# Performance work log

Measured on AMD Instinct MI355X. Metric: run time of the kernel, lower is better.

Reference implementation:

```python
import jax, jax.numpy as jnp
import numpy as np

B, TE, TD, H, D = 8, 2048, 256, 128, 128


def setup_inputs() -> dict:
    key = jax.random.key(0)
    k1, k2, k3, k4, k5 = jax.random.split(key, 5)
    he = lambda k, shape: jax.random.normal(k, shape, dtype=jnp.float32) * jnp.sqrt(2.0 / shape[0])
    return {
        "encoder_out_seq": jax.random.normal(k1, (B, TE, H), dtype=jnp.float32),
        "decoder_out_seq": jax.random.normal(k2, (B, TD, D), dtype=jnp.float32),
        "W_a": he(k3, (H, H)),
        "U_a": he(k4, (D, H)),
        "V_a": he(k5, (H, 1)),
    }


def reference(encoder_out_seq, decoder_out_seq, W_a, U_a, V_a):
    # Precompute encoder and decoder projections once (the TF code redundantly
    # recomputes enc@W_a every decoder step inside backend.rnn).
    Wenc = jnp.einsum('bth,hk->btk', encoder_out_seq, W_a)      # [B,Te,H]
    Udec = jnp.einsum('bjd,dk->bjk', decoder_out_seq, U_a)     # [B,Td,H]
    # Additive (Bahdanau) scores: v^T tanh(W s_i + U h_j)
    scores = jnp.einsum('bjtk,k->bjt',
                        jnp.tanh(Wenc[:, None, :, :] + Udec[:, :, None, :]),
                        V_a[:, 0])                              # [B,Td,Te]
    e_outputs = jax.nn.softmax(scores, axis=-1)                 # [B,Td,Te]
    c_outputs = jnp.einsum('bjt,bth->bjh', e_outputs, encoder_out_seq)  # [B,Td,H]
    return c_outputs, e_outputs
```

## Files before the change

kernel.cpp:

```cpp
#include <hip/hip_runtime.h>
#include <stdint.h>

#define B  8
#define TE 2048
#define TD 256
#define H  128

#define FMA4(acc, s, wv) \
  acc.x += (s)*(wv).x; acc.y += (s)*(wv).y; acc.z += (s)*(wv).z; acc.w += (s)*(wv).w

__global__ __launch_bounds__(256) void proj_kernel(
    const float* __restrict__ enc, const float* __restrict__ dec,
    const float* __restrict__ Wa,  const float* __restrict__ Ua,
    float* __restrict__ EgT, float* __restrict__ Fg) {
  __shared__ float Ls[16 * 132];
  const float C2 = 2.8853900817779268f;
  int tid = threadIdx.x;
  int bid = blockIdx.x;
  bool isE = (bid < 1024);
  int rbase = (isE ? bid : bid - 1024) * 16;
  const float* in = isE ? enc : dec;
  const float* Mg = isE ? Wa : Ua;
  int hq = tid & 31, rq = tid >> 5;
  int h0 = hq * 4, r0 = rq * 2;
  const float* rowp = in + (size_t)(rbase + r0) * H;
  const float* wp = Mg + h0;
  float4 a0{0,0,0,0}, a1{0,0,0,0};
  #pragma unroll 2
  for (int kb = 0; kb < 32; ++kb) {
    float4 rv0 = *(const float4*)(rowp + kb * 4);
    float4 rv1 = *(const float4*)(rowp + H + kb * 4);
    float4 w0 = *(const float4*)(wp + (size_t)(4 * kb + 0) * H);
    float4 w1 = *(const float4*)(wp + (size_t)(4 * kb + 1) * H);
    float4 w2 = *(const float4*)(wp + (size_t)(4 * kb + 2) * H);
    float4 w3 = *(const float4*)(wp + (size_t)(4 * kb + 3) * H);
    FMA4(a0, rv0.x, w0); FMA4(a0, rv0.y, w1); FMA4(a0, rv0.z, w2); FMA4(a0, rv0.w, w3);
    FMA4(a1, rv1.x, w0); FMA4(a1, rv1.y, w1); FMA4(a1, rv1.z, w2); FMA4(a1, rv1.w, w3);
  }
  float4 e0, e1;
  e0.x = __builtin_amdgcn_exp2f(a0.x * C2); e0.y = __builtin_amdgcn_exp2f(a0.y * C2);
  e0.z = __builtin_amdgcn_exp2f(a0.z * C2); e0.w = __builtin_amdgcn_exp2f(a0.w * C2);
  e1.x = __builtin_amdgcn_exp2f(a1.x * C2); e1.y = __builtin_amdgcn_exp2f(a1.y * C2);
  e1.z = __builtin_amdgcn_exp2f(a1.z * C2); e1.w = __builtin_amdgcn_exp2f(a1.w * C2);
  if (isE) {
    *(float4*)&Ls[(r0 + 0) * 132 + h0] = e0;
    *(float4*)&Ls[(r0 + 1) * 132 + h0] = e1;
    __syncthreads();
    int b_e = rbase >> 11, t_in = rbase & 2047;
    int tb = t_in >> 6, toff = t_in & 63;
    float* dst = EgT + ((size_t)(b_e * 32 + tb) * 128) * 64 + toff;
    #pragma unroll
    for (int jj = 0; jj < 8; ++jj) {
      int idx = jj * 256 + tid;
      int r = idx & 15, k = idx >> 4;
      dst[(size_t)k * 64 + r] = Ls[r * 132 + k];
    }
  } else {
    int b_f = rbase >> 8, j_in = rbase & 255;
    float* dst = Fg + ((size_t)(b_f * TD + j_in + r0)) * H + h0;
    *(float4*)(dst + 0 * H) = e0;
    *(float4*)(dst + 1 * H) = e1;
  }
}

__global__ __launch_bounds__(512, 4) void fused_kernel(
    const float* __restrict__ EgT, const float* __restrict__ Fg,
    const float* __restrict__ Va,  const float* __restrict__ enc,
    float* __restrict__ oute, float* __restrict__ outc) {
  __shared__ float S[4 * 2048];
  __shared__ float red[16];
  int tid = threadIdx.x;
  int bid = blockIdx.x;
  int b = bid & 7, jt = bid >> 3;
  int j0 = jt * 4;
  int lane = tid & 63, w = tid >> 6;
  const float4* vp = (const float4*)Va;
  float V1 = 0.f;
  #pragma unroll
  for (int q = 0; q < 32; ++q) { float4 v = vp[q]; V1 += v.x + v.y + v.z + v.w; }

  const float4* Fp = (const float4*)(Fg + (size_t)(b * TD + j0) * H);
  const float* Ep[4];
  #pragma unroll
  for (int it = 0; it < 4; ++it)
    Ep[it] = EgT + ((size_t)(b * 32 + w + 8 * it) * 128) * 64 + lane;
  float s[4][4];
  #pragma unroll
  for (int it = 0; it < 4; ++it)
    #pragma unroll
    for (int j = 0; j < 4; ++j) s[it][j] = 0.f;

  for (int kc = 0; kc < 16; ++kc) {
    float4 f0[4], f1[4];
    const float4* fpc = Fp + kc * 2;
    #pragma unroll
    for (int j = 0; j < 4; ++j) {
      f0[j] = fpc[j * 32];
      f1[j] = fpc[j * 32 + 1];
    }
    float4 v0 = vp[kc * 2], v1 = vp[kc * 2 + 1];
    #pragma unroll
    for (int it = 0; it < 4; ++it) {
      const float* ep = Ep[it] + kc * 512;
      float ek[8];
      #pragma unroll
      for (int q = 0; q < 8; ++q) ek[q] = ep[q * 64];
      #pragma unroll
      for (int j = 0; j < 4; ++j) {
        float d0, d1, a = 0.f;
        d0 = fmaf(ek[0], f0[j].x, 1.0f); d1 = fmaf(ek[1], f0[j].y, 1.0f);
        a += (v0.x * d1 + v0.y * d0) * __builtin_amdgcn_rcpf(d0 * d1);
        d0 = fmaf(ek[2], f0[j].z, 1.0f); d1 = fmaf(ek[3], f0[j].w, 1.0f);
        a += (v0.z * d1 + v0.w * d0) * __builtin_amdgcn_rcpf(d0 * d1);
        d0 = fmaf(ek[4], f1[j].x, 1.0f); d1 = fmaf(ek[5], f1[j].y, 1.0f);
        a += (v1.x * d1 + v1.y * d0) * __builtin_amdgcn_rcpf(d0 * d1);
        d0 = fmaf(ek[6], f1[j].z, 1.0f); d1 = fmaf(ek[7], f1[j].w, 1.0f);
        a += (v1.z * d1 + v1.w * d0) * __builtin_amdgcn_rcpf(d0 * d1);
        s[it][j] += a;
      }
    }
  }
  #pragma unroll
  for (int it = 0; it < 4; ++it) {
    int t = (w + 8 * it) * 64 + lane;
    S[0 * 2048 + t] = V1 - 2.0f * s[it][0];
    S[1 * 2048 + t] = V1 - 2.0f * s[it][1];
    S[2 * 2048 + t] = V1 - 2.0f * s[it][2];
    S[3 * 2048 + t] = V1 - 2.0f * s[it][3];
  }
  __syncthreads();

  int j = w >> 1, half = w & 1;
  int tb2 = half * 1024 + lane;
  float x[16];
  #pragma unroll
  for (int q = 0; q < 16; ++q) x[q] = S[j * 2048 + tb2 + q * 64];
  float m = x[0];
  #pragma unroll
  for (int q = 1; q < 16; ++q) m = fmaxf(m, x[q]);
  #pragma unroll
  for (int off = 32; off > 0; off >>= 1) m = fmaxf(m, __shfl_xor(m, off));
  if (lane == 0) red[w] = m;
  __syncthreads();
  m = fmaxf(red[j * 2], red[j * 2 + 1]);
  const float L2E = 1.4426950408889634f;
  float sum = 0.f;
  #pragma unroll
  for (int q = 0; q < 16; ++q) {
    x[q] = __builtin_amdgcn_exp2f((x[q] - m) * L2E);
    sum += x[q];
  }
  #pragma unroll
  for (int off = 32; off > 0; off >>= 1) sum += __shfl_xor(sum, off);
  if (lane == 0) red[8 + w] = sum;
  __syncthreads();
  float inv = 1.0f / (red[8 + j * 2] + red[8 + j * 2 + 1]);
  float* orow = oute + (size_t)(b * TD + j0 + j) * TE;
  #pragma unroll
  for (int q = 0; q < 16; ++q) {
    float e = x[q] * inv;
    int t = tb2 + q * 64;
    orow[t] = e;
    S[t * 4 + j] = e;
  }
  __syncthreads();

  int hq = tid & 31, slice = tid >> 5;
  const float* encp = enc + ((size_t)b * TE + slice * 128) * H + hq * 4;
  float4 acc0{0,0,0,0}, acc1{0,0,0,0}, acc2{0,0,0,0}, acc3{0,0,0,0};
  #pragma unroll 4
  for (int t = 0; t < 128; ++t) {
    float4 ev = *(const float4*)(encp + (size_t)t * H);
    float4 e4 = *(const float4*)&S[(slice * 128 + t) * 4];
    acc0.x += e4.x * ev.x; acc0.y += e4.x * ev.y; acc0.z += e4.x * ev.z; acc0.w += e4.x * ev.w;
    acc1.x += e4.y * ev.x; acc1.y += e4.y * ev.y; acc1.z += e4.y * ev.z; acc1.w += e4.y * ev.w;
    acc2.x += e4.z * ev.x; acc2.y += e4.z * ev.y; acc2.z += e4.z * ev.z; acc2.w += e4.z * ev.w;
    acc3.x += e4.w * ev.x; acc3.y += e4.w * ev.y; acc3.z += e4.w * ev.z; acc3.w += e4.w * ev.w;
  }
  __syncthreads();
  *(float4*)&S[slice * 512 + 0 * 128 + hq * 4] = acc0;
  *(float4*)&S[slice * 512 + 1 * 128 + hq * 4] = acc1;
  *(float4*)&S[slice * 512 + 2 * 128 + hq * 4] = acc2;
  *(float4*)&S[slice * 512 + 3 * 128 + hq * 4] = acc3;
  __syncthreads();
  float r = 0.f;
  #pragma unroll
  for (int sl = 0; sl < 16; ++sl) r += S[sl * 512 + tid];
  outc[(size_t)(b * TD + j0 + (tid >> 7)) * H + (tid & 127)] = r;
}

extern "C" void kernel_launch(void* const* d_in, const int* in_sizes, int n_in,
                              void* d_out, int out_size, void* d_ws, size_t ws_size,
                              hipStream_t stream) {
  (void)in_sizes; (void)n_in; (void)out_size; (void)ws_size;
  const float* enc = (const float*)d_in[0];
  const float* dec = (const float*)d_in[1];
  const float* Wa  = (const float*)d_in[2];
  const float* Ua  = (const float*)d_in[3];
  const float* Va  = (const float*)d_in[4];

  float* ws  = (float*)d_ws;
  float* EgT = ws;
  float* Fg  = EgT + (size_t)B * TE * H;
  float* outc = (float*)d_out;
  float* oute = outc + (size_t)B * TD * H;

  proj_kernel<<<dim3(1152), 256, 0, stream>>>(enc, dec, Wa, Ua, EgT, Fg);
  fused_kernel<<<dim3(512), 512, 0, stream>>>(EgT, Fg, Va, enc, oute, outc);
}
```

Before: 168.8 us.

## Process eight decoder rows per block with 1024 threads in fused attention kernel

```diff
diff --git a/kernel.cpp b/kernel.cpp
--- a/kernel.cpp
+++ b/kernel.cpp
@@ -63,16 +63,16 @@
   }
 }
 
-__global__ __launch_bounds__(512, 4) void fused_kernel(
+__global__ __launch_bounds__(1024, 4) void fused_kernel(
     const float* __restrict__ EgT, const float* __restrict__ Fg,
     const float* __restrict__ Va,  const float* __restrict__ enc,
     float* __restrict__ oute, float* __restrict__ outc) {
-  __shared__ float S[4 * 2048];
-  __shared__ float red[16];
+  __shared__ float S[8 * 2048];
+  __shared__ float red[32];
   int tid = threadIdx.x;
   int bid = blockIdx.x;
   int b = bid & 7, jt = bid >> 3;
-  int j0 = jt * 4;
+  int j0 = jt * 8;
   int lane = tid & 63, w = tid >> 6;
   const float4* vp = (const float4*)Va;
   float V1 = 0.f;
@@ -80,53 +80,56 @@
   for (int q = 0; q < 32; ++q) { float4 v = vp[q]; V1 += v.x + v.y + v.z + v.w; }
 
   const float4* Fp = (const float4*)(Fg + (size_t)(b * TD + j0) * H);
-  const float* Ep[4];
-  #pragma unroll
-  for (int it = 0; it < 4; ++it)
-    Ep[it] = EgT + ((size_t)(b * 32 + w + 8 * it) * 128) * 64 + lane;
-  float s[4][4];
-  #pragma unroll
-  for (int it = 0; it < 4; ++it)
-    #pragma unroll
-    for (int j = 0; j < 4; ++j) s[it][j] = 0.f;
+  const float* Ep0 = EgT + ((size_t)(b * 32 + w) * 128) * 64 + lane;
+  const float* Ep1 = EgT + ((size_t)(b * 32 + w + 16) * 128) * 64 + lane;
+  float s0[8], s1[8];
+  #pragma unroll
+  for (int j = 0; j < 8; ++j) { s0[j] = 0.f; s1[j] = 0.f; }
+
+#define UNIT(acc, ekk, jj)                                                \
+  {                                                                       \
+    float d0, d1, a = 0.f;                                                \
+    d0 = fmaf(ekk[0], f0[jj].x, 1.0f); d1 = fmaf(ekk[1], f0[jj].y, 1.0f); \
+    a += (v0.x * d1 + v0.y * d0) * __builtin_amdgcn_rcpf(d0 * d1);        \
+    d0 = fmaf(ekk[2], f0[jj].z, 1.0f); d1 = fmaf(ekk[3], f0[jj].w, 1.0f); \
+    a += (v0.z * d1 + v0.w * d0) * __builtin_amdgcn_rcpf(d0 * d1);        \
+    d0 = fmaf(ekk[4], f1[jj].x, 1.0f); d1 = fmaf(ekk[5], f1[jj].y, 1.0f); \
+    a += (v1.x * d1 + v1.y * d0) * __builtin_amdgcn_rcpf(d0 * d1);        \
+    d0 = fmaf(ekk[6], f1[jj].z, 1.0f); d1 = fmaf(ekk[7], f1[jj].w, 1.0f); \
+    a += (v1.z * d1 + v1.w * d0) * __builtin_amdgcn_rcpf(d0 * d1);        \
+    acc[jj] += a;                                                         \
+  }
 
   for (int kc = 0; kc < 16; ++kc) {
-    float4 f0[4], f1[4];
+    float4 f0[8], f1[8];
     const float4* fpc = Fp + kc * 2;
     #pragma unroll
-    for (int j = 0; j < 4; ++j) {
+    for (int j = 0; j < 8; ++j) {
       f0[j] = fpc[j * 32];
       f1[j] = fpc[j * 32 + 1];
     }
     float4 v0 = vp[kc * 2], v1 = vp[kc * 2 + 1];
-    #pragma unroll
-    for (int it = 0; it < 4; ++it) {
-      const float* ep = Ep[it] + kc * 512;
+    {
+      const float* ep = Ep0 + kc * 512;
       float ek[8];
       #pragma unroll
       for (int q = 0; q < 8; ++q) ek[q] = ep[q * 64];
       #pragma unroll
-      for (int j = 0; j < 4; ++j) {
-        float d0, d1, a = 0.f;
-        d0 = fmaf(ek[0], f0[j].x, 1.0f); d1 = fmaf(ek[1], f0[j].y, 1.0f);
-        a += (v0.x * d1 + v0.y * d0) * __builtin_amdgcn_rcpf(d0 * d1);
-        d0 = fmaf(ek[2], f0[j].z, 1.0f); d1 = fmaf(ek[3], f0[j].w, 1.0f);
-        a += (v0.z * d1 + v0.w * d0) * __builtin_amdgcn_rcpf(d0 * d1);
-        d0 = fmaf(ek[4], f1[j].x, 1.0f); d1 = fmaf(ek[5], f1[j].y, 1.0f);
-        a += (v1.x * d1 + v1.y * d0) * __builtin_amdgcn_rcpf(d0 * d1);
-        d0 = fmaf(ek[6], f1[j].z, 1.0f); d1 = fmaf(ek[7], f1[j].w, 1.0f);
-        a += (v1.z * d1 + v1.w * d0) * __builtin_amdgcn_rcpf(d0 * d1);
-        s[it][j] += a;
-      }
-    }
-  }
-  #pragma unroll
-  for (int it = 0; it < 4; ++it) {
-    int t = (w + 8 * it) * 64 + lane;
-    S[0 * 2048 + t] = V1 - 2.0f * s[it][0];
-    S[1 * 2048 + t] = V1 - 2.0f * s[it][1];
-    S[2 * 2048 + t] = V1 - 2.0f * s[it][2];
-    S[3 * 2048 + t] = V1 - 2.0f * s[it][3];
+      for (int j = 0; j < 8; ++j) UNIT(s0, ek, j)
+    }
+    {
+      const float* ep = Ep1 + kc * 512;
+      float ek[8];
+      #pragma unroll
+      for (int q = 0; q < 8; ++q) ek[q] = ep[q * 64];
+      #pragma unroll
+      for (int j = 0; j < 8; ++j) UNIT(s1, ek, j)
+    }
+  }
+  #pragma unroll
+  for (int j = 0; j < 8; ++j) {
+    S[j * 2048 + w * 64 + lane]        = V1 - 2.0f * s0[j];
+    S[j * 2048 + (w + 16) * 64 + lane] = V1 - 2.0f * s1[j];
   }
   __syncthreads();
 
@@ -152,40 +155,56 @@
   }
   #pragma unroll
   for (int off = 32; off > 0; off >>= 1) sum += __shfl_xor(sum, off);
-  if (lane == 0) red[8 + w] = sum;
-  __syncthreads();
-  float inv = 1.0f / (red[8 + j * 2] + red[8 + j * 2 + 1]);
+  if (lane == 0) red[16 + w] = sum;
+  __syncthreads();
+  float inv = 1.0f / (red[16 + j * 2] + red[16 + j * 2 + 1]);
   float* orow = oute + (size_t)(b * TD + j0 + j) * TE;
   #pragma unroll
   for (int q = 0; q < 16; ++q) {
     float e = x[q] * inv;
     int t = tb2 + q * 64;
     orow[t] = e;
-    S[t * 4 + j] = e;
+    S[j * 2048 + t] = e;
   }
   __syncthreads();
 
   int hq = tid & 31, slice = tid >> 5;
-  const float* encp = enc + ((size_t)b * TE + slice * 128) * H + hq * 4;
-  float4 acc0{0,0,0,0}, acc1{0,0,0,0}, acc2{0,0,0,0}, acc3{0,0,0,0};
-  #pragma unroll 4
-  for (int t = 0; t < 128; ++t) {
+  const float* encp = enc + ((size_t)b * TE + slice * 64) * H + hq * 4;
+  const float* Se = S + slice * 64;
+  float4 ac0{0,0,0,0}, ac1{0,0,0,0}, ac2{0,0,0,0}, ac3{0,0,0,0};
+  float4 ac4{0,0,0,0}, ac5{0,0,0,0}, ac6{0,0,0,0}, ac7{0,0,0,0};
+  #pragma unroll 2
+  for (int t = 0; t < 64; ++t) {
     float4 ev = *(const float4*)(encp + (size_t)t * H);
-    float4 e4 = *(const float4*)&S[(slice * 128 + t) * 4];
-    acc0.x += e4.x * ev.x; acc0.y += e4.x * ev.y; acc0.z += e4.x * ev.z; acc0.w += e4.x * ev.w;
-    acc1.x += e4.y * ev.x; acc1.y += e4.y * ev.y; acc1.z += e4.y * ev.z; acc1.w += e4.y * ev.w;
-    acc2.x += e4.z * ev.x; acc2.y += e4.z * ev.y; acc2.z += e4.z * ev.z; acc2.w += e4.z * ev.w;
-    acc3.x += e4.w * ev.x; acc3.y += e4.w * ev.y; acc3.z += e4.w * ev.z; acc3.w += e4.w * ev.w;
-  }
-  __syncthreads();
-  *(float4*)&S[slice * 512 + 0 * 128 + hq * 4] = acc0;
-  *(float4*)&S[slice * 512 + 1 * 128 + hq * 4] = acc1;
-  *(float4*)&S[slice * 512 + 2 * 128 + hq * 4] = acc2;
-  *(float4*)&S[slice * 512 + 3 * 128 + hq * 4] = acc3;
+    float e0v = Se[0 * 2048 + t], e1v = Se[1 * 2048 + t];
+    float e2v = Se[2 * 2048 + t], e3v = Se[3 * 2048 + t];
+    float e4v = Se[4 * 2048 + t], e5v = Se[5 * 2048 + t];
+    float e6v = Se[6 * 2048 + t], e7v = Se[7 * 2048 + t];
+    FMA4(ac0, e0v, ev); FMA4(ac1, e1v, ev); FMA4(ac2, e2v, ev); FMA4(ac3, e3v, ev);
+    FMA4(ac4, e4v, ev); FMA4(ac5, e5v, ev); FMA4(ac6, e6v, ev); FMA4(ac7, e7v, ev);
+  }
+  __syncthreads();
+  if (slice < 16) {
+    float* dst = &S[slice * 1024 + hq * 4];
+    *(float4*)(dst + 0 * 128) = ac0; *(float4*)(dst + 1 * 128) = ac1;
+    *(float4*)(dst + 2 * 128) = ac2; *(float4*)(dst + 3 * 128) = ac3;
+    *(float4*)(dst + 4 * 128) = ac4; *(float4*)(dst + 5 * 128) = ac5;
+    *(float4*)(dst + 6 * 128) = ac6; *(float4*)(dst + 7 * 128) = ac7;
+  }
+  __syncthreads();
+  if (slice >= 16) {
+    float* dst = &S[(slice - 16) * 1024 + hq * 4];
+    #define RMW(J, AC) { float4 p = *(float4*)(dst + J * 128); \
+      p.x += AC.x; p.y += AC.y; p.z += AC.z; p.w += AC.w; \
+      *(float4*)(dst + J * 128) = p; }
+    RMW(0, ac0) RMW(1, ac1) RMW(2, ac2) RMW(3, ac3)
+    RMW(4, ac4) RMW(5, ac5) RMW(6, ac6) RMW(7, ac7)
+    #undef RMW
+  }
   __syncthreads();
   float r = 0.f;
   #pragma unroll
-  for (int sl = 0; sl < 16; ++sl) r += S[sl * 512 + tid];
+  for (int sl = 0; sl < 16; ++sl) r += S[sl * 1024 + tid];
   outc[(size_t)(b * TD + j0 + (tid >> 7)) * H + (tid & 127)] = r;
 }
 
@@ -206,5 +225,5 @@
   float* oute = outc + (size_t)B * TD * H;
 
   proj_kernel<<<dim3(1152), 256, 0, stream>>>(enc, dec, Wa, Ua, EgT, Fg);
-  fused_kernel<<<dim3(512), 512, 0, stream>>>(EgT, Fg, Va, enc, oute, outc);
+  fused_kernel<<<dim3(256), 1024, 0, stream>>>(EgT, Fg, Va, enc, oute, outc);
 }
```

Measured after the change: 169.9 us. Within noise of the previous version (+0.6%).

## Prefetch encoder tiles, merge reciprocals, and restructure context accumulation layout

Applied to the files above, without the earlier changes.

```diff
diff --git a/kernel.cpp b/kernel.cpp
--- a/kernel.cpp
+++ b/kernel.cpp
@@ -89,7 +89,26 @@
   for (int it = 0; it < 4; ++it)
     #pragma unroll
     for (int j = 0; j < 4; ++j) s[it][j] = 0.f;
-
+  float eka[8], ekb[8];
+
+#define LOADE(dst, base, off)                                        \
+  { const float* _p = (base) + (off);                                \
+    dst[0] = _p[0];   dst[1] = _p[64];  dst[2] = _p[128];            \
+    dst[3] = _p[192]; dst[4] = _p[256]; dst[5] = _p[320];            \
+    dst[6] = _p[384]; dst[7] = _p[448]; }
+
+#define UNIT4(accres, e0_, e1_, e2_, e3_, fv, vv)                         \
+  {                                                                       \
+    float d0 = fmaf(e0_, fv.x, 1.0f), d1 = fmaf(e1_, fv.y, 1.0f);        \
+    float d2 = fmaf(e2_, fv.z, 1.0f), d3 = fmaf(e3_, fv.w, 1.0f);        \
+    float p01 = d0 * d1, p23 = d2 * d3;                                   \
+    float rP = __builtin_amdgcn_rcpf(p01 * p23);                          \
+    float n01 = vv.x * d1 + vv.y * d0;                                    \
+    float n23 = vv.z * d3 + vv.w * d2;                                    \
+    accres = fmaf(n01 * p23 + n23 * p01, rP, accres);                     \
+  }
+
+  LOADE(eka, Ep[0], 0);
   for (int kc = 0; kc < 16; ++kc) {
     float4 f0[4], f1[4];
     const float4* fpc = Fp + kc * 2;
@@ -101,23 +120,15 @@
     float4 v0 = vp[kc * 2], v1 = vp[kc * 2 + 1];
     #pragma unroll
     for (int it = 0; it < 4; ++it) {
-      const float* ep = Ep[it] + kc * 512;
-      float ek[8];
-      #pragma unroll
-      for (int q = 0; q < 8; ++q) ek[q] = ep[q * 64];
+      if (it < 3) { LOADE(ekb, Ep[it + 1], kc * 512); }
+      else        { LOADE(ekb, Ep[0], (kc + 1) * 512); }
       #pragma unroll
       for (int j = 0; j < 4; ++j) {
-        float d0, d1, a = 0.f;
-        d0 = fmaf(ek[0], f0[j].x, 1.0f); d1 = fmaf(ek[1], f0[j].y, 1.0f);
-        a += (v0.x * d1 + v0.y * d0) * __builtin_amdgcn_rcpf(d0 * d1);
-        d0 = fmaf(ek[2], f0[j].z, 1.0f); d1 = fmaf(ek[3], f0[j].w, 1.0f);
-        a += (v0.z * d1 + v0.w * d0) * __builtin_amdgcn_rcpf(d0 * d1);
-        d0 = fmaf(ek[4], f1[j].x, 1.0f); d1 = fmaf(ek[5], f1[j].y, 1.0f);
-        a += (v1.x * d1 + v1.y * d0) * __builtin_amdgcn_rcpf(d0 * d1);
-        d0 = fmaf(ek[6], f1[j].z, 1.0f); d1 = fmaf(ek[7], f1[j].w, 1.0f);
-        a += (v1.z * d1 + v1.w * d0) * __builtin_amdgcn_rcpf(d0 * d1);
-        s[it][j] += a;
+        UNIT4(s[it][j], eka[0], eka[1], eka[2], eka[3], f0[j], v0);
+        UNIT4(s[it][j], eka[4], eka[5], eka[6], eka[7], f1[j], v1);
       }
+      #pragma unroll
+      for (int q = 0; q < 8; ++q) eka[q] = ekb[q];
     }
   }
   #pragma unroll
@@ -161,31 +172,61 @@
     float e = x[q] * inv;
     int t = tb2 + q * 64;
     orow[t] = e;
-    S[t * 4 + j] = e;
+    S[j * 2048 + t] = e;
   }
   __syncthreads();
 
   int hq = tid & 31, slice = tid >> 5;
   const float* encp = enc + ((size_t)b * TE + slice * 128) * H + hq * 4;
-  float4 acc0{0,0,0,0}, acc1{0,0,0,0}, acc2{0,0,0,0}, acc3{0,0,0,0};
-  #pragma unroll 4
-  for (int t = 0; t < 128; ++t) {
-    float4 ev = *(const float4*)(encp + (size_t)t * H);
-    float4 e4 = *(const float4*)&S[(slice * 128 + t) * 4];
-    acc0.x += e4.x * ev.x; acc0.y += e4.x * ev.y; acc0.z += e4.x * ev.z; acc0.w += e4.x * ev.w;
-    acc1.x += e4.y * ev.x; acc1.y += e4.y * ev.y; acc1.z += e4.y * ev.z; acc1.w += e4.y * ev.w;
-    acc2.x += e4.z * ev.x; acc2.y += e4.z * ev.y; acc2.z += e4.z * ev.z; acc2.w += e4.z * ev.w;
-    acc3.x += e4.w * ev.x; acc3.y += e4.w * ev.y; acc3.z += e4.w * ev.z; acc3.w += e4.w * ev.w;
-  }
-  __syncthreads();
-  *(float4*)&S[slice * 512 + 0 * 128 + hq * 4] = acc0;
-  *(float4*)&S[slice * 512 + 1 * 128 + hq * 4] = acc1;
-  *(float4*)&S[slice * 512 + 2 * 128 + hq * 4] = acc2;
-  *(float4*)&S[slice * 512 + 3 * 128 + hq * 4] = acc3;
+  const float* Se = S + slice * 128;
+  float4 ac0{0,0,0,0}, ac1{0,0,0,0}, ac2{0,0,0,0}, ac3{0,0,0,0};
+  float4 evA0, evA1, evA2, evA3, evB0, evB1, evB2, evB3;
+
+#define LOADENC(d0, d1, d2, d3, t0)                         \
+  d0 = *(const float4*)(encp + (size_t)(t0 + 0) * H);       \
+  d1 = *(const float4*)(encp + (size_t)(t0 + 1) * H);       \
+  d2 = *(const float4*)(encp + (size_t)(t0 + 2) * H);       \
+  d3 = *(const float4*)(encp + (size_t)(t0 + 3) * H);
+
+#define GROUP(t0, ex, ey, ez, ew)                                            \
+  {                                                                          \
+    float4 E0 = *(const float4*)&Se[0 * 2048 + (t0)];                        \
+    float4 E1 = *(const float4*)&Se[1 * 2048 + (t0)];                        \
+    float4 E2 = *(const float4*)&Se[2 * 2048 + (t0)];                        \
+    float4 E3 = *(const float4*)&Se[3 * 2048 + (t0)];                        \
+    FMA4(ac0, E0.x, ex); FMA4(ac0, E0.y, ey); FMA4(ac0, E0.z, ez); FMA4(ac0, E0.w, ew); \
+    FMA4(ac1, E1.x, ex); FMA4(ac1, E1.y, ey); FMA4(ac1, E1.z, ez); FMA4(ac1, E1.w, ew); \
+    FMA4(ac2, E2.x, ex); FMA4(ac2, E2.y, ey); FMA4(ac2, E2.z, ez); FMA4(ac2, E2.w, ew); \
+    FMA4(ac3, E3.x, ex); FMA4(ac3, E3.y, ey); FMA4(ac3, E3.z, ez); FMA4(ac3, E3.w, ew); \
+  }
+
+  LOADENC(evA0, evA1, evA2, evA3, 0);
+  #pragma unroll
+  for (int tb = 0; tb < 128; tb += 8) {
+    LOADENC(evB0, evB1, evB2, evB3, tb + 4);
+    GROUP(tb, evA0, evA1, evA2, evA3);
+    if (tb < 120) { LOADENC(evA0, evA1, evA2, evA3, tb + 8); }
+    GROUP(tb + 4, evB0, evB1, evB2, evB3);
+  }
+  __syncthreads();
+  if (slice < 8) {
+    float* dst = &S[slice * 512 + hq * 4];
+    *(float4*)(dst + 0 * 128) = ac0; *(float4*)(dst + 1 * 128) = ac1;
+    *(float4*)(dst + 2 * 128) = ac2; *(float4*)(dst + 3 * 128) = ac3;
+  }
+  __syncthreads();
+  if (slice >= 8) {
+    float* dst = &S[(slice - 8) * 512 + hq * 4];
+    #define RMW(J, AC) { float4 p = *(float4*)(dst + J * 128); \
+      p.x += AC.x; p.y += AC.y; p.z += AC.z; p.w += AC.w; \
+      *(float4*)(dst + J * 128) = p; }
+    RMW(0, ac0) RMW(1, ac1) RMW(2, ac2) RMW(3, ac3)
+    #undef RMW
+  }
   __syncthreads();
   float r = 0.f;
   #pragma unroll
-  for (int sl = 0; sl < 16; ++sl) r += S[sl * 512 + tid];
+  for (int sl = 0; sl < 8; ++sl) r += S[sl * 512 + tid];
   outc[(size_t)(b * TD + j0 + (tid >> 7)) * H + (tid & 127)] = r;
 }
 
```

Result: slower. 176.0 us (+4.2%).
